# Optimization experiments

Hardware: AMD Instinct MI355X
Metric: run time of the kernel (lower is better)

Reference implementation:

```python
import jax, jax.numpy as jnp
import numpy as np

NG, N, NFG, NFR, NFP, B = 4, 64, 1024, 256, 256, 2048
SCALE = 1.0 / float(np.sqrt(NFR + NFP))
EPS = 1e-5  # torch LayerNorm default


def setup_inputs() -> dict:
    key = jax.random.key(0)
    k = jax.random.split(key, 4)
    x = jax.random.normal(k[0], (B, N, NFG), dtype=jnp.float32)
    # per-graph params stacked over NG for vectorized computation
    Wt = jax.random.normal(k[1], (NG, NFR, NFG), dtype=jnp.float32) * 0.02
    bt = jnp.zeros((NG, NFR), dtype=jnp.float32)
    Wp = jax.random.normal(k[2], (NG, NFR, NFG), dtype=jnp.float32) * 0.02
    bp = jnp.zeros((NG, NFR), dtype=jnp.float32)
    Wg = jax.random.normal(k[3], (NG, NFG, NFG), dtype=jnp.float32) * 0.02  # [out,in]
    gamma = jnp.ones((NG, NFG), dtype=jnp.float32)
    beta = jnp.zeros((NG, NFG), dtype=jnp.float32)
    return {"x": x, "Wt": Wt, "bt": bt, "Wp": Wp, "bp": bp,
            "Wg": Wg, "gamma": gamma, "beta": beta}


def reference(x, Wt, bt, Wp, bp, Wg, gamma, beta):
    # theta/phi projections, vectorized over NG graphs: [G,B,N,R]
    theta = jnp.einsum('bnf,grf->gbnr', x, Wt) + bt[:, None, None, :]
    phi = jnp.einsum('bnf,grf->gbnr', x, Wp) + bp[:, None, None, :]
    # original computes sim=theta@phi^T then .sum(2); identical math:
    # relation[b,n] = theta[b,n] . sum_m phi[b,m]  (avoids the NxN matrix)
    phi_sum = phi.sum(axis=2)                                  # [G,B,R]
    relation = jnp.einsum('gbnr,gbr->gbn', theta, phi_sum) * SCALE
    w = jax.nn.softmax(relation, axis=2)                       # softmax over boxes N
    # attention-weighted aggregation over boxes -> [G,B,NFG]
    agg = jnp.einsum('gbn,bnf->gbf', w, x)
    # GCN linear (no bias): [G,B,NFG]
    h = jnp.einsum('gbf,gof->gbo', agg, Wg)
    # LayerNorm over feature dim, per graph
    mu = h.mean(axis=-1, keepdims=True)
    var = ((h - mu) ** 2).mean(axis=-1, keepdims=True)
    h = (h - mu) * jax.lax.rsqrt(var + EPS) * gamma[:, None, :] + beta[:, None, :]
    h = jax.nn.relu(h)
    # mean over the NG graphs; restore keepdim axis -> [B,1,NFG]
    return h.mean(axis=0)[:, None, :]
```

## Files before the change

### kernel.cpp

```cpp
#include <hip/hip_runtime.h>
#include <hip/hip_bf16.h>

typedef __attribute__((ext_vector_type(4))) float f4;
typedef __attribute__((ext_vector_type(4))) float f32x4;
typedef __attribute__((ext_vector_type(8))) short short8;
typedef __attribute__((ext_vector_type(2))) unsigned int u32x2;
typedef __attribute__((ext_vector_type(4))) unsigned int u32x4;
typedef unsigned int u32;
typedef unsigned short u16;

#define SCALE_F 0.04419417382415922f

__device__ inline u16 f2bf(float f) {
  u32 u = __float_as_uint(f);
  u32 r = u + 0x7FFFu + ((u >> 16) & 1u);
  return (u16)(r >> 16);
}
__device__ inline u32 pk(float a, float b) {
  return (u32)f2bf(a) | ((u32)f2bf(b) << 16);
}
__device__ inline float bflo(u32 u) { return __uint_as_float(u << 16); }
__device__ inline float bfhi(u32 u) { return __uint_as_float(u & 0xFFFF0000u); }

#define GLD16(gsrc, ldst)                                                     \
  __builtin_amdgcn_global_load_lds(                                           \
      (const __attribute__((address_space(1))) void*)(gsrc),                  \
      (__attribute__((address_space(3))) void*)(ldst), 16, 0, 0)

#define SWZ(o) (((o) & ~2047) | (((((o) >> 4) & 127) ^ (((o) >> 11) & 7)) << 4))

__device__ __forceinline__ void cvt8(const float* __restrict__ src,
                                     u16* __restrict__ dst, int blk, int t) {
  int i = blk * 256 + t;
  const f4* s = (const f4*)src;
  f4 a = s[(size_t)i * 2];
  f4 b = s[(size_t)i * 2 + 1];
  u32x4 p;
  p[0] = pk(a[0], a[1]);
  p[1] = pk(a[2], a[3]);
  p[2] = pk(b[0], b[1]);
  p[3] = pk(b[2], b[3]);
  *(u32x4*)(dst + (size_t)i * 8) = p;
}

__global__ __launch_bounds__(256) void k01_prep(const float* __restrict__ x,
                                                const float* __restrict__ Wg,
                                                const float* __restrict__ Wp,
                                                const float* __restrict__ Wt,
                                                u16* __restrict__ xs16,
                                                char* __restrict__ xpre,
                                                u16* __restrict__ wgb,
                                                u16* __restrict__ wpb,
                                                u16* __restrict__ wtb) {
  __shared__ float red[256][8];
  __shared__ u16 tile[64][66];
  const int blk = blockIdx.x, t = threadIdx.x;
  if (blk < 2048) {
    const int b = blk;
    const float* xb = x + (size_t)b * 65536;
    char* xp = xpre + (size_t)b * 131072;
    const int g16 = t & 127, rp = t >> 7;
    f4 acc0 = {0.f, 0.f, 0.f, 0.f}, acc1 = {0.f, 0.f, 0.f, 0.f};
#pragma unroll 8
    for (int it = 0; it < 32; ++it) {
      int n = it * 2 + rp;
      const float* src = xb + n * 1024 + g16 * 8;
      f4 v0 = *(const f4*)(src);
      f4 v1 = *(const f4*)(src + 4);
      acc0 += v0;
      acc1 += v1;
      u32x4 p;
      p[0] = pk(v0[0], v0[1]);
      p[1] = pk(v0[2], v0[3]);
      p[2] = pk(v1[0], v1[1]);
      p[3] = pk(v1[2], v1[3]);
      *(u32x4*)(xp + n * 2048 + g16 * 16) = p;
    }
    *(f4*)&red[t][0] = acc0;
    *(f4*)&red[t][4] = acc1;
    __syncthreads();
    if (t < 128) {
      f4 s0 = *(const f4*)&red[t][0];
      f4 s1 = *(const f4*)&red[t][4];
      f4 q0 = *(const f4*)&red[t + 128][0];
      f4 q1 = *(const f4*)&red[t + 128][4];
      s0 += q0;
      s1 += q1;
      u32x4 p;
      p[0] = pk(s0[0], s0[1]);
      p[1] = pk(s0[2], s0[3]);
      p[2] = pk(s1[0], s1[1]);
      p[3] = pk(s1[2], s1[3]);
      *(u32x4*)(xs16 + (size_t)b * 1024 + t * 8) = p;
    }
  } else if (blk < 4096) {
    cvt8(Wg, wgb, blk - 2048, t);
  } else if (blk < 4608) {
    cvt8(Wp, wpb, blk - 4096, t);
  } else {
    const int bid = blk - 4608;
    const int g = bid >> 6, rem = bid & 63;
    const int f0 = (rem & 15) * 64, r0 = (rem >> 4) * 64;
    const float* src = Wt + ((size_t)g * 256 + r0) * 1024 + f0;
#pragma unroll
    for (int i = 0; i < 16; ++i) {
      int idx = t + i * 256;
      int rl = idx >> 6, fl = idx & 63;
      tile[fl][rl] = f2bf(src[rl * 1024 + fl]);
    }
    __syncthreads();
    u16* dst = wtb + ((size_t)g * 1024 + f0) * 256 + r0;
#pragma unroll
    for (int i = 0; i < 4; ++i) {
      int idx = t + i * 256;
      int fl = idx >> 4, rq = idx & 15;
      u32x2 p;
      p[0] = (u32)tile[fl][rq * 4]     | ((u32)tile[fl][rq * 4 + 1] << 16);
      p[1] = (u32)tile[fl][rq * 4 + 2] | ((u32)tile[fl][rq * 4 + 3] << 16);
      *(u32x2*)(dst + fl * 256 + rq * 4) = p;
    }
  }
}

__global__ __launch_bounds__(256) void k2_gemm(const u16* __restrict__ A,
                                               const u16* __restrict__ Bt,
                                               const float* __restrict__ bp,
                                               u16* __restrict__ C) {
  const int n0 = blockIdx.x * 64, m0 = blockIdx.y * 128;
  __shared__ u16 Al[128 * 32];
  __shared__ u16 Bl[64 * 32];
  const int t = threadIdx.x;
  const int w = t >> 6, l = t & 63;
  const int lr = l & 15, lh = l >> 4;
  f32x4 acc[2][4] = {};
  for (int kt = 0; kt < 1024; kt += 32) {
#pragma unroll
    for (int j = 0; j < 2; ++j) {
      int idx = t + j * 256;
      int row = idx >> 2, sl = idx & 3;
      GLD16(A + (size_t)(m0 + row) * 1024 + kt + sl * 8, Al + idx * 8);
    }
    {
      int row = t >> 2, sl = t & 3;
      GLD16(Bt + (size_t)(n0 + row) * 1024 + kt + sl * 8, Bl + t * 8);
    }
    __syncthreads();
    short8 af[2], bfr[4];
#pragma unroll
    for (int m = 0; m < 2; ++m)
      af[m] = *(const short8*)(Al + (w * 32 + m * 16 + lr) * 32 + lh * 8);
#pragma unroll
    for (int n = 0; n < 4; ++n)
      bfr[n] = *(const short8*)(Bl + (n * 16 + lr) * 32 + lh * 8);
#pragma unroll
    for (int m = 0; m < 2; ++m)
#pragma unroll
      for (int n = 0; n < 4; ++n)
        acc[m][n] = __builtin_amdgcn_mfma_f32_16x16x32_bf16(af[m], bfr[n],
                                                            acc[m][n], 0, 0, 0);
    __syncthreads();
  }
#pragma unroll
  for (int m = 0; m < 2; ++m)
#pragma unroll
    for (int n = 0; n < 4; ++n) {
      int col = n0 + n * 16 + lr;
      float bb = 64.0f * bp[col];
#pragma unroll
      for (int j = 0; j < 4; ++j)
        C[(size_t)(m0 + w * 32 + m * 16 + lh * 4 + j) * 1024 + col] =
            f2bf(acc[m][n][j] + bb);
    }
}

__global__ __launch_bounds__(256) void k3_gemm(const u16* __restrict__ A,
                                               const u16* __restrict__ Btt,
                                               u16* __restrict__ Vb) {
  const int id = blockIdx.x;
  const int wg = (id & 7) * 64 + (id >> 3);
  const int n0 = (wg & 7) * 128, m0 = ((wg >> 3) & 15) * 128, g = wg >> 7;
  const u16* Bg = Btt + (size_t)g * 1024 * 256;
  __shared__ u16 Al[128 * 64];
  __shared__ u16 Bl[128 * 64];
  const int t = threadIdx.x;
  const int w = t >> 6, l = t & 63;
  const int wr = w >> 1, wc = w & 1;
  const int lr = l & 15, lh = l >> 4;
  f32x4 acc[4][4] = {};
  for (int kt = 0; kt < 256; kt += 64) {
#pragma unroll
    for (int j = 0; j < 4; ++j) {
      int idx = t + j * 256;
      int row = idx >> 3, sl = idx & 7;
      int ssl = sl ^ (row & 7);
      GLD16(A + (size_t)(m0 + row) * 1024 + g * 256 + kt + ssl * 8,
            Al + idx * 8);
      GLD16(Bg + (size_t)(n0 + row) * 256 + kt + ssl * 8, Bl + idx * 8);
    }
    __syncthreads();
    short8 af[4][2], bfr[4][2];
#pragma unroll
    for (int m = 0; m < 4; ++m) {
      int row = wr * 64 + m * 16 + lr;
#pragma unroll
      for (int ks = 0; ks < 2; ++ks)
        af[m][ks] =
            *(const short8*)(Al + row * 64 + (((ks * 4 + lh) ^ (row & 7)) * 8));
    }
#pragma unroll
    for (int n = 0; n < 4; ++n) {
      int row = wc * 64 + n * 16 + lr;
#pragma unroll
      for (int ks = 0; ks < 2; ++ks)
        bfr[n][ks] =
            *(const short8*)(Bl + row * 64 + (((ks * 4 + lh) ^ (row & 7)) * 8));
    }
#pragma unroll
    for (int m = 0; m < 4; ++m)
#pragma unroll
      for (int n = 0; n < 4; ++n) {
        acc[m][n] = __builtin_amdgcn_mfma_f32_16x16x32_bf16(
            af[m][0], bfr[n][0], acc[m][n], 0, 0, 0);
        acc[m][n] = __builtin_amdgcn_mfma_f32_16x16x32_bf16(
            af[m][1], bfr[n][1], acc[m][n], 0, 0, 0);
      }
    __syncthreads();
  }
  u16* Vg = Vb + (size_t)g * 2048 * 1024;
#pragma unroll
  for (int m = 0; m < 4; ++m)
#pragma unroll
    for (int n = 0; n < 4; ++n)
#pragma unroll
      for (int j = 0; j < 4; ++j)
        Vg[(size_t)(m0 + wr * 64 + m * 16 + lh * 4 + j) * 1024 +
           (n0 + wc * 64 + n * 16 + lr)] = f2bf(acc[m][n][j]);
}

__device__ __forceinline__ void relation_phase(const char* xl, const u16* vb,
                                               float* relp, int w, int l) {
  const int lg = l >> 4, lr = l & 15;
  f32x4 racc[4] = {};
#pragma unroll
  for (int kp = 0; kp < 2; ++kp) {
    const int kt = kp * 512 + w * 32;
    short8 afr = {};
    if (lr < 4) afr = *(const short8*)(vb + lr * 1032 + kt + lg * 8);
#pragma unroll
    for (int nt = 0; nt < 4; ++nt) {
      int n = nt * 16 + lr;
      short8 bfrg = *(const short8*)(
          xl + n * 2048 + ((((kt >> 3) + lg) ^ (n & 7)) << 4));
      racc[nt] = __builtin_amdgcn_mfma_f32_16x16x32_bf16(afr, bfrg, racc[nt],
                                                         0, 0, 0);
    }
  }
  if (l < 16) {
#pragma unroll
    for (int nt = 0; nt < 4; ++nt)
#pragma unroll
      for (int j = 0; j < 4; ++j)
        relp[(w * 4 + j) * 64 + nt * 16 + lr] = racc[nt][j];
  }
}

__device__ __forceinline__ void softmax_phase(const float* relp, float* wsm,
                                              int t) {
  if (t < 256) {
    const int g = t >> 6, n = t & 63;
    float rel = 0.f;
#pragma unroll
    for (int ww = 0; ww < 16; ++ww) rel += relp[(ww * 4 + g) * 64 + n];
    rel *= SCALE_F;
    float mx = rel;
#pragma unroll
    for (int o = 32; o > 0; o >>= 1) mx = fmaxf(mx, __shfl_xor(mx, o, 64));
    float e = __expf(rel - mx);
    float s = e;
#pragma unroll
    for (int o = 32; o > 0; o >>= 1) s += __shfl_xor(s, o, 64);
    wsm[t] = e / s;
  }
}

__device__ __forceinline__ void agg_phase(const char* xl, const float* wsm,
                                          float* relp, u16* aggb, int b,
                                          int t) {
  const int hh = t >> 9, r = t & 511, g = r >> 7, f8 = r & 127;
  const float* wg = wsm + g * 64 + hh * 32;
  float a0 = 0, a1 = 0, a2 = 0, a3 = 0, a4 = 0, a5 = 0, a6 = 0, a7 = 0;
#pragma unroll 8
  for (int n0 = 0; n0 < 32; ++n0) {
    int n = hh * 32 + n0;
    float wv = wg[n0];
    u32x4 xp = *(const u32x4*)(xl + n * 2048 + ((f8 ^ (n & 7)) << 4));
    a0 = fmaf(bflo(xp[0]), wv, a0);
    a1 = fmaf(bfhi(xp[0]), wv, a1);
    a2 = fmaf(bflo(xp[1]), wv, a2);
    a3 = fmaf(bfhi(xp[1]), wv, a3);
    a4 = fmaf(bflo(xp[2]), wv, a4);
    a5 = fmaf(bfhi(xp[2]), wv, a5);
    a6 = fmaf(bflo(xp[3]), wv, a6);
    a7 = fmaf(bfhi(xp[3]), wv, a7);
  }
  if (hh) {
    f4 q0 = {a0, a1, a2, a3};
    f4 q1 = {a4, a5, a6, a7};
    *(f4*)(relp + r * 8) = q0;
    *(f4*)(relp + r * 8 + 4) = q1;
  }
  __syncthreads();
  if (!hh) {
    f4 q0 = *(const f4*)(relp + r * 8);
    f4 q1 = *(const f4*)(relp + r * 8 + 4);
    u32x4 p;
    p[0] = pk(a0 + q0[0], a1 + q0[1]);
    p[1] = pk(a2 + q0[2], a3 + q0[3]);
    p[2] = pk(a4 + q1[0], a5 + q1[1]);
    p[3] = pk(a6 + q1[2], a7 + q1[3]);
    *(u32x4*)(aggb + ((size_t)g * 2048 + b) * 1024 + f8 * 8) = p;
  }
}

#define K4_LDS (131072 + 8256 + 16384 + 1024)
__global__ __launch_bounds__(1024) void k4_fused(const char* __restrict__ xpre,
                                                 const u16* __restrict__ vb16,
                                                 u16* __restrict__ aggb) {
  extern __shared__ char sm[];
  char* xl = sm;
  u16* vb = (u16*)(sm + 131072);
  float* relp = (float*)(sm + 131072 + 8256);
  float* wsm = (float*)(sm + 131072 + 8256 + 16384);
  const int t = threadIdx.x;
  const int w = t >> 6, l = t & 63;
  const int bbase = (255 - (int)blockIdx.x) * 8;

  {
    int g = t >> 8, q = t & 255;
    u32x2 pv = *(const u32x2*)(vb16 + ((size_t)g * 2048 + bbase) * 1024 + q * 4);
    *(u32x2*)(vb + g * 1032 + q * 4) = pv;
  }
  const char* xg0 = xpre + (size_t)bbase * 131072;
#pragma unroll
  for (int i = 0; i < 8; ++i) {
    int o = (w * 8 + i) * 1024 + l * 16;
    GLD16(xg0 + SWZ(o), xl + o);
  }
  __syncthreads();

  u32x4 pf0, pf1, pf2, pf3, pf4, pf5, pf6, pf7;
  u32x2 pv1;
  for (int ib = 0; ib < 8; ++ib) {
    const int b = bbase + ib;
    if (ib < 7) {
      const char* xg1 = xpre + (size_t)(b + 1) * 131072;
      pf0 = *(const u32x4*)(xg1 + SWZ(t * 16));
      pf1 = *(const u32x4*)(xg1 + SWZ(t * 16 + 16384));
      pf2 = *(const u32x4*)(xg1 + SWZ(t * 16 + 32768));
      pf3 = *(const u32x4*)(xg1 + SWZ(t * 16 + 49152));
      pf4 = *(const u32x4*)(xg1 + SWZ(t * 16 + 65536));
      pf5 = *(const u32x4*)(xg1 + SWZ(t * 16 + 81920));
      pf6 = *(const u32x4*)(xg1 + SWZ(t * 16 + 98304));
      pf7 = *(const u32x4*)(xg1 + SWZ(t * 16 + 114688));
      pv1 = *(const u32x2*)(vb16 + ((size_t)(t >> 8) * 2048 + (b + 1)) * 1024 +
                            (t & 255) * 4);
    }
    relation_phase(xl, vb, relp, w, l);
    __syncthreads();
    softmax_phase(relp, wsm, t);
    __syncthreads();
    agg_phase(xl, wsm, relp, aggb, b, t);
    __syncthreads();
    if (ib < 7) {
      *(u32x4*)(xl + t * 16) = pf0;
      *(u32x4*)(xl + t * 16 + 16384) = pf1;
      *(u32x4*)(xl + t * 16 + 32768) = pf2;
      *(u32x4*)(xl + t * 16 + 49152) = pf3;
      *(u32x4*)(xl + t * 16 + 65536) = pf4;
      *(u32x4*)(xl + t * 16 + 81920) = pf5;
      *(u32x4*)(xl + t * 16 + 98304) = pf6;
      *(u32x4*)(xl + t * 16 + 114688) = pf7;
      *(u32x2*)(vb + (t >> 8) * 1032 + (t & 255) * 4) = pv1;
      __syncthreads();
    }
  }
}

__global__ __launch_bounds__(256) void k5_gemm(const u16* __restrict__ Ab,
                                               const u16* __restrict__ Bb,
                                               u16* __restrict__ H) {
  const int id = blockIdx.x;
  const int wg = (id & 7) * 64 + (id >> 3);
  const int n0 = (wg & 7) * 128, m0 = ((wg >> 3) & 15) * 128, g = wg >> 7;
  const u16* A = Ab + (size_t)g * 2048 * 1024;
  const u16* Bt = Bb + (size_t)g * 1024 * 1024;
  __shared__ u16 Al[128 * 64];
  __shared__ u16 Bl[128 * 64];
  const int t = threadIdx.x;
  const int w = t >> 6, l = t & 63;
  const int wr = w >> 1, wc = w & 1;
  const int lr = l & 15, lh = l >> 4;
  f32x4 acc[4][4] = {};
  for (int kt = 0; kt < 1024; kt += 64) {
#pragma unroll
    for (int j = 0; j < 4; ++j) {
      int idx = t + j * 256;
      int row = idx >> 3, sl = idx & 7;
      int ssl = sl ^ (row & 7);
      GLD16(A + (size_t)(m0 + row) * 1024 + kt + ssl * 8, Al + idx * 8);
      GLD16(Bt + (size_t)(n0 + row) * 1024 + kt + ssl * 8, Bl + idx * 8);
    }
    __syncthreads();
    short8 af[4][2], bfr[4][2];
#pragma unroll
    for (int m = 0; m < 4; ++m) {
      int row = wr * 64 + m * 16 + lr;
#pragma unroll
      for (int ks = 0; ks < 2; ++ks)
        af[m][ks] =
            *(const short8*)(Al + row * 64 + (((ks * 4 + lh) ^ (row & 7)) * 8));
    }
#pragma unroll
    for (int n = 0; n < 4; ++n) {
      int row = wc * 64 + n * 16 + lr;
#pragma unroll
      for (int ks = 0; ks < 2; ++ks)
        bfr[n][ks] =
            *(const short8*)(Bl + row * 64 + (((ks * 4 + lh) ^ (row & 7)) * 8));
    }
#pragma unroll
    for (int m = 0; m < 4; ++m)
#pragma unroll
      for (int n = 0; n < 4; ++n) {
        acc[m][n] = __builtin_amdgcn_mfma_f32_16x16x32_bf16(
            af[m][0], bfr[n][0], acc[m][n], 0, 0, 0);
        acc[m][n] = __builtin_amdgcn_mfma_f32_16x16x32_bf16(
            af[m][1], bfr[n][1], acc[m][n], 0, 0, 0);
      }
    __syncthreads();
  }
  u16* Hg = H + (size_t)g * 2048 * 1024;
#pragma unroll
  for (int m = 0; m < 4; ++m)
#pragma unroll
    for (int n = 0; n < 4; ++n)
#pragma unroll
      for (int j = 0; j < 4; ++j)
        Hg[(size_t)(m0 + wr * 64 + m * 16 + lh * 4 + j) * 1024 +
           (n0 + wc * 64 + n * 16 + lr)] = f2bf(acc[m][n][j]);
}

__global__ __launch_bounds__(256) void k6_ln(const u16* __restrict__ H,
                                             const float* __restrict__ gamma,
                                             const float* __restrict__ beta,
                                             float* __restrict__ out) {
  const int b = blockIdx.x, t = threadIdx.x;
  const int w = t >> 6, lane = t & 63;
  __shared__ float red[8];
  f4 acc = {0.f, 0.f, 0.f, 0.f};
  for (int g = 0; g < 4; ++g) {
    u32x2 hp = *(const u32x2*)(H + ((size_t)g * 2048 + b) * 1024 + t * 4);
    f4 hv = {bflo(hp[0]), bfhi(hp[0]), bflo(hp[1]), bfhi(hp[1])};
    float s = hv[0] + hv[1] + hv[2] + hv[3];
    float q = hv[0] * hv[0] + hv[1] * hv[1] + hv[2] * hv[2] + hv[3] * hv[3];
#pragma unroll
    for (int o = 32; o > 0; o >>= 1) {
      s += __shfl_xor(s, o, 64);
      q += __shfl_xor(q, o, 64);
    }
    if (lane == 0) { red[w] = s; red[4 + w] = q; }
    __syncthreads();
    s = red[0] + red[1] + red[2] + red[3];
    q = red[4] + red[5] + red[6] + red[7];
    float mean = s * (1.f / 1024.f);
    float var = q * (1.f / 1024.f) - mean * mean;
    float rstd = rsqrtf(var + 1e-5f);
    f4 gm = *(const f4*)(gamma + g * 1024 + t * 4);
    f4 bt = *(const f4*)(beta + g * 1024 + t * 4);
#pragma unroll
    for (int j = 0; j < 4; ++j) {
      float val = (hv[j] - mean) * rstd * gm[j] + bt[j];
      acc[j] += fmaxf(val, 0.f);
    }
    __syncthreads();
  }
  acc *= 0.25f;
  *(f4*)(out + (size_t)b * 1024 + t * 4) = acc;
}

extern "C" void kernel_launch(void* const* d_in, const int* in_sizes, int n_in,
                              void* d_out, int out_size, void* d_ws, size_t ws_size,
                              hipStream_t stream) {
  const float* x     = (const float*)d_in[0];
  const float* Wt    = (const float*)d_in[1];
  const float* Wp    = (const float*)d_in[3];
  const float* bp    = (const float*)d_in[4];
  const float* Wg    = (const float*)d_in[5];
  const float* gamma = (const float*)d_in[6];
  const float* beta  = (const float*)d_in[7];
  float* out = (float*)d_out;

  char* ws = (char*)d_ws;
  u16*   xs16 = (u16*)(ws);
  u16*   ps16 = (u16*)(ws + (4u << 20));
  u16*   wpb  = (u16*)(ws + (8u << 20));
  u16*   wtb  = (u16*)(ws + (10u << 20));
  u16*   wgb  = (u16*)(ws + (12u << 20));
  u16*   vb16 = (u16*)(ws + (20u << 20));
  u16*   aggb = (u16*)(ws + (36u << 20));
  u16*   hb16 = (u16*)(ws + (52u << 20));
  char*  xpre = (char*)(ws + (68u << 20));

  hipFuncSetAttribute((const void*)k4_fused,
                      hipFuncAttributeMaxDynamicSharedMemorySize, K4_LDS);

  k01_prep<<<4864, 256, 0, stream>>>(x, Wg, Wp, Wt, xs16, xpre, wgb, wpb, wtb);
  k2_gemm<<<dim3(16, 16), 256, 0, stream>>>(xs16, wpb, bp, ps16);
  k3_gemm<<<512, 256, 0, stream>>>(ps16, wtb, vb16);
  k4_fused<<<256, 1024, K4_LDS, stream>>>(xpre, vb16, aggb);
  k5_gemm<<<512, 256, 0, stream>>>(aggb, wgb, hb16);
  k6_ln<<<2048, 256, 0, stream>>>(hb16, gamma, beta, out);
}
```

Baseline: 308.1 us.

## Double-buffer LDS tiles in the three GEMM kernels to overlap loads with MFMA

Adds a second LDS buffer to k2, k3 and k5. The global-to-LDS loads for the next K tile are issued before the MFMA work on the current tile, with explicit vmcnt waits and raw s_barrier in place of __syncthreads. The goal is to hide global load latency behind matrix math. It doubles shared memory per block, which can lower occupancy, and it relies on hand-counted vmcnt values and the ordering of the asm barriers being correct.

After: 309.0 us. Within noise of the previous version (+0.3%).

```diff
diff --git a/kernel.cpp b/kernel.cpp
--- a/kernel.cpp
+++ b/kernel.cpp
@@ -127,39 +127,54 @@
                                                const float* __restrict__ bp,
                                                u16* __restrict__ C) {
   const int n0 = blockIdx.x * 64, m0 = blockIdx.y * 128;
-  __shared__ u16 Al[128 * 32];
-  __shared__ u16 Bl[64 * 32];
+  __shared__ u16 Al[2][128 * 32];
+  __shared__ u16 Bl[2][64 * 32];
   const int t = threadIdx.x;
   const int w = t >> 6, l = t & 63;
   const int lr = l & 15, lh = l >> 4;
   f32x4 acc[2][4] = {};
-  for (int kt = 0; kt < 1024; kt += 32) {
-#pragma unroll
-    for (int j = 0; j < 2; ++j) {
-      int idx = t + j * 256;
-      int row = idx >> 2, sl = idx & 3;
-      GLD16(A + (size_t)(m0 + row) * 1024 + kt + sl * 8, Al + idx * 8);
-    }
-    {
-      int row = t >> 2, sl = t & 3;
-      GLD16(Bt + (size_t)(n0 + row) * 1024 + kt + sl * 8, Bl + t * 8);
-    }
-    __syncthreads();
+
+#define K2_STAGE(buf, kt)                                                     \
+  do {                                                                        \
+    _Pragma("unroll") for (int j = 0; j < 2; ++j) {                           \
+      int idx = t + j * 256;                                                  \
+      int row = idx >> 2, sl = idx & 3;                                       \
+      GLD16(A + (size_t)(m0 + row) * 1024 + (kt) + sl * 8,                    \
+            Al[buf] + idx * 8);                                               \
+    }                                                                         \
+    {                                                                         \
+      int row = t >> 2, sl = t & 3;                                           \
+      GLD16(Bt + (size_t)(n0 + row) * 1024 + (kt) + sl * 8, Bl[buf] + t * 8); \
+    }                                                                         \
+  } while (0)
+
+  K2_STAGE(0, 0);
+  int cur = 0;
+  for (int s = 0; s < 32; ++s) {
+    if (s < 31) {
+      K2_STAGE(cur ^ 1, (s + 1) * 32);
+      asm volatile("s_waitcnt vmcnt(3)" ::: "memory");
+    } else {
+      asm volatile("s_waitcnt vmcnt(0)" ::: "memory");
+    }
+    __builtin_amdgcn_s_barrier();
     short8 af[2], bfr[4];
 #pragma unroll
     for (int m = 0; m < 2; ++m)
-      af[m] = *(const short8*)(Al + (w * 32 + m * 16 + lr) * 32 + lh * 8);
+      af[m] = *(const short8*)(Al[cur] + (w * 32 + m * 16 + lr) * 32 + lh * 8);
 #pragma unroll
     for (int n = 0; n < 4; ++n)
-      bfr[n] = *(const short8*)(Bl + (n * 16 + lr) * 32 + lh * 8);
+      bfr[n] = *(const short8*)(Bl[cur] + (n * 16 + lr) * 32 + lh * 8);
 #pragma unroll
     for (int m = 0; m < 2; ++m)
 #pragma unroll
       for (int n = 0; n < 4; ++n)
         acc[m][n] = __builtin_amdgcn_mfma_f32_16x16x32_bf16(af[m], bfr[n],
                                                             acc[m][n], 0, 0, 0);
-    __syncthreads();
-  }
+    __builtin_amdgcn_s_barrier();
+    cur ^= 1;
+  }
+#undef K2_STAGE
 #pragma unroll
   for (int m = 0; m < 2; ++m)
 #pragma unroll
@@ -180,40 +195,53 @@
   const int wg = (id & 7) * 64 + (id >> 3);
   const int n0 = (wg & 7) * 128, m0 = ((wg >> 3) & 15) * 128, g = wg >> 7;
   const u16* Bg = Btt + (size_t)g * 1024 * 256;
-  __shared__ u16 Al[128 * 64];
-  __shared__ u16 Bl[128 * 64];
+  __shared__ u16 Al[2][128 * 64];
+  __shared__ u16 Bl[2][128 * 64];
   const int t = threadIdx.x;
   const int w = t >> 6, l = t & 63;
   const int wr = w >> 1, wc = w & 1;
   const int lr = l & 15, lh = l >> 4;
   f32x4 acc[4][4] = {};
-  for (int kt = 0; kt < 256; kt += 64) {
-#pragma unroll
-    for (int j = 0; j < 4; ++j) {
-      int idx = t + j * 256;
-      int row = idx >> 3, sl = idx & 7;
-      int ssl = sl ^ (row & 7);
-      GLD16(A + (size_t)(m0 + row) * 1024 + g * 256 + kt + ssl * 8,
-            Al + idx * 8);
-      GLD16(Bg + (size_t)(n0 + row) * 256 + kt + ssl * 8, Bl + idx * 8);
-    }
-    __syncthreads();
+
+#define K3_STAGE(buf, kt)                                                     \
+  do {                                                                        \
+    _Pragma("unroll") for (int j = 0; j < 4; ++j) {                           \
+      int idx = t + j * 256;                                                  \
+      int row = idx >> 3, sl = idx & 7;                                       \
+      int ssl = sl ^ (row & 7);                                               \
+      GLD16(A + (size_t)(m0 + row) * 1024 + g * 256 + (kt) + ssl * 8,         \
+            Al[buf] + idx * 8);                                               \
+      GLD16(Bg + (size_t)(n0 + row) * 256 + (kt) + ssl * 8,                   \
+            Bl[buf] + idx * 8);                                               \
+    }                                                                         \
+  } while (0)
+
+  K3_STAGE(0, 0);
+  int cur = 0;
+  for (int s = 0; s < 4; ++s) {
+    if (s < 3) {
+      K3_STAGE(cur ^ 1, (s + 1) * 64);
+      asm volatile("s_waitcnt vmcnt(8)" ::: "memory");
+    } else {
+      asm volatile("s_waitcnt vmcnt(0)" ::: "memory");
+    }
+    __builtin_amdgcn_s_barrier();
     short8 af[4][2], bfr[4][2];
 #pragma unroll
     for (int m = 0; m < 4; ++m) {
       int row = wr * 64 + m * 16 + lr;
 #pragma unroll
       for (int ks = 0; ks < 2; ++ks)
-        af[m][ks] =
-            *(const short8*)(Al + row * 64 + (((ks * 4 + lh) ^ (row & 7)) * 8));
+        af[m][ks] = *(const short8*)(Al[cur] + row * 64 +
+                                     (((ks * 4 + lh) ^ (row & 7)) * 8));
     }
 #pragma unroll
     for (int n = 0; n < 4; ++n) {
       int row = wc * 64 + n * 16 + lr;
 #pragma unroll
       for (int ks = 0; ks < 2; ++ks)
-        bfr[n][ks] =
-            *(const short8*)(Bl + row * 64 + (((ks * 4 + lh) ^ (row & 7)) * 8));
+        bfr[n][ks] = *(const short8*)(Bl[cur] + row * 64 +
+                                      (((ks * 4 + lh) ^ (row & 7)) * 8));
     }
 #pragma unroll
     for (int m = 0; m < 4; ++m)
@@ -224,8 +252,10 @@
         acc[m][n] = __builtin_amdgcn_mfma_f32_16x16x32_bf16(
             af[m][1], bfr[n][1], acc[m][n], 0, 0, 0);
       }
-    __syncthreads();
-  }
+    __builtin_amdgcn_s_barrier();
+    cur ^= 1;
+  }
+#undef K3_STAGE
   u16* Vg = Vb + (size_t)g * 2048 * 1024;
 #pragma unroll
   for (int m = 0; m < 4; ++m)
@@ -394,39 +424,53 @@
   const int n0 = (wg & 7) * 128, m0 = ((wg >> 3) & 15) * 128, g = wg >> 7;
   const u16* A = Ab + (size_t)g * 2048 * 1024;
   const u16* Bt = Bb + (size_t)g * 1024 * 1024;
-  __shared__ u16 Al[128 * 64];
-  __shared__ u16 Bl[128 * 64];
+  __shared__ u16 Al[2][128 * 64];
+  __shared__ u16 Bl[2][128 * 64];
   const int t = threadIdx.x;
   const int w = t >> 6, l = t & 63;
   const int wr = w >> 1, wc = w & 1;
   const int lr = l & 15, lh = l >> 4;
   f32x4 acc[4][4] = {};
-  for (int kt = 0; kt < 1024; kt += 64) {
-#pragma unroll
-    for (int j = 0; j < 4; ++j) {
-      int idx = t + j * 256;
-      int row = idx >> 3, sl = idx & 7;
-      int ssl = sl ^ (row & 7);
-      GLD16(A + (size_t)(m0 + row) * 1024 + kt + ssl * 8, Al + idx * 8);
-      GLD16(Bt + (size_t)(n0 + row) * 1024 + kt + ssl * 8, Bl + idx * 8);
-    }
-    __syncthreads();
+
+#define K5_STAGE(buf, kt)                                                     \
+  do {                                                                        \
+    _Pragma("unroll") for (int j = 0; j < 4; ++j) {                           \
+      int idx = t + j * 256;                                                  \
+      int row = idx >> 3, sl = idx & 7;                                       \
+      int ssl = sl ^ (row & 7);                                               \
+      GLD16(A + (size_t)(m0 + row) * 1024 + (kt) + ssl * 8,                   \
+            Al[buf] + idx * 8);                                               \
+      GLD16(Bt + (size_t)(n0 + row) * 1024 + (kt) + ssl * 8,                  \
+            Bl[buf] + idx * 8);                                               \
+    }                                                                         \
+  } while (0)
+
+  K5_STAGE(0, 0);
+  int cur = 0;
+  for (int s = 0; s < 16; ++s) {
+    if (s < 15) {
+      K5_STAGE(cur ^ 1, (s + 1) * 64);
+      asm volatile("s_waitcnt vmcnt(8)" ::: "memory");
+    } else {
+      asm volatile("s_waitcnt vmcnt(0)" ::: "memory");
+    }
+    __builtin_amdgcn_s_barrier();
     short8 af[4][2], bfr[4][2];
 #pragma unroll
     for (int m = 0; m < 4; ++m) {
       int row = wr * 64 + m * 16 + lr;
 #pragma unroll
       for (int ks = 0; ks < 2; ++ks)
-        af[m][ks] =
-            *(const short8*)(Al + row * 64 + (((ks * 4 + lh) ^ (row & 7)) * 8));
+        af[m][ks] = *(const short8*)(Al[cur] + row * 64 +
+                                     (((ks * 4 + lh) ^ (row & 7)) * 8));
     }
 #pragma unroll
     for (int n = 0; n < 4; ++n) {
       int row = wc * 64 + n * 16 + lr;
 #pragma unroll
       for (int ks = 0; ks < 2; ++ks)
-        bfr[n][ks] =
-            *(const short8*)(Bl + row * 64 + (((ks * 4 + lh) ^ (row & 7)) * 8));
+        bfr[n][ks] = *(const short8*)(Bl[cur] + row * 64 +
+                                      (((ks * 4 + lh) ^ (row & 7)) * 8));
     }
 #pragma unroll
     for (int m = 0; m < 4; ++m)
@@ -437,8 +481,10 @@
         acc[m][n] = __builtin_amdgcn_mfma_f32_16x16x32_bf16(
             af[m][1], bfr[n][1], acc[m][n], 0, 0, 0);
       }
-    __syncthreads();
-  }
+    __builtin_amdgcn_s_barrier();
+    cur ^= 1;
+  }
+#undef K5_STAGE
   u16* Hg = H + (size_t)g * 2048 * 1024;
 #pragma unroll
   for (int m = 0; m < 4; ++m)
```
